# Kernel optimization log

Measured on AMD Instinct MI355X. Metric: run time of the kernel, lower is better.

Reference implementation:

```python
import jax, jax.numpy as jnp
import numpy as np

D, N, H, DK, DFF, L = 1024, 2048, 8, 128, 4096, 4
LAM = 1.0 / float(np.sqrt(DK))  # attention scale (layer.lam)


def setup_inputs() -> dict:
    key = jax.random.key(0)
    ks = jax.random.split(key, 6)
    s = 1.0 / float(np.sqrt(D))
    X = jax.random.normal(ks[0], (D, N), jnp.float32)
    Q = jax.random.normal(ks[1], (L, H, DK, D), jnp.float32) * s
    K = jax.random.normal(ks[2], (L, H, DK, D), jnp.float32) * s
    V = jax.random.normal(ks[3], (L, H, D, D), jnp.float32) * s
    W1 = jax.random.normal(ks[4], (L, DFF, D), jnp.float32) * s
    b1 = jnp.zeros((L, DFF, 1), jnp.float32)
    W2 = jax.random.normal(ks[5], (L, D, DFF), jnp.float32) * (1.0 / float(np.sqrt(DFF)))
    b2 = jnp.zeros((L, D, 1), jnp.float32)
    return {"X": X, "Q": Q, "K": K, "V": V, "W1": W1, "b1": b1, "W2": W2, "b2": b2}


def _layer(X, p):
    Q, K, V, W1, b1, W2, b2 = p
    # Batched multi-head attention; original loops heads and sums outputs.
    QX = jnp.einsum('hkd,dn->hkn', Q, X)          # [H, DK, N]
    KX = jnp.einsum('hkd,dn->hkn', K, X)          # [H, DK, N]
    scores = jnp.einsum('hkn,hkm->hnm', QX, KX) * LAM  # [H, N, N]
    A = jax.nn.softmax(scores, axis=1)            # torch softmax(dim=0) over [N, N]
    VX = jnp.einsum('hed,dn->hen', V, X)          # [H, D, N]
    Y = jnp.einsum('hen,hnm->em', VX, A)          # sum over heads -> [D, N]
    X = X + Y
    Hh = jax.nn.relu(W1 @ X + b1)                 # [DFF, N]
    return X + W2 @ Hh + b2


def reference(X, Q, K, V, W1, b1, W2, b2):
    def step(carry, p):
        return _layer(carry, p), None
    Xf, _ = jax.lax.scan(step, X, (Q, K, V, W1, b1, W2, b2))
    return Xf
```

## Files before the change

### kernel.cpp

```cpp
#include <hip/hip_runtime.h>

typedef unsigned short u16;
typedef _Float16 f16;
typedef _Float16 fh8 __attribute__((ext_vector_type(8)));
typedef float f32x4 __attribute__((ext_vector_type(4)));

#define cD   1024
#define cN   2048
#define cH   8
#define cDK  128
#define cDFF 4096
#define cL   4
#define LAM_ 0.08838834764831845f
#define QKSC 64.0f

__device__ __forceinline__ u16 f2h(float f) {
    union { f16 h; u16 u; } x; x.h = (f16)f; return x.u;
}
__device__ __forceinline__ float h2f(u16 u) {
    union { u16 u; f16 h; } x; x.u = u; return (float)x.h;
}
__device__ __forceinline__ void split_fh(float v, u16& h, u16& l) {
    h = f2h(v);
    l = f2h(v - h2f(h));
}

__device__ __forceinline__ void async_cp16(const u16* gsrc, u16* ldst) {
    __builtin_amdgcn_global_load_lds(
        (const __attribute__((address_space(1))) unsigned int*)gsrc,
        (__attribute__((address_space(3))) unsigned int*)(unsigned int)(unsigned long long)ldst,
        16, 0, 0);
}

__global__ void cast_split4(const float* __restrict__ s, u16* __restrict__ h,
                            u16* __restrict__ l, int n4, float sc) {
    int i = blockIdx.x * 256 + threadIdx.x;
    if (i < n4) {
        float4 v = ((const float4*)s)[i];
        v.x *= sc; v.y *= sc; v.z *= sc; v.w *= sc;
        ushort4 hh, ll;
        split_fh(v.x, hh.x, ll.x);
        split_fh(v.y, hh.y, ll.y);
        split_fh(v.z, hh.z, ll.z);
        split_fh(v.w, hh.w, ll.w);
        ((ushort4*)h)[i] = hh;
        if (l) ((ushort4*)l)[i] = ll;
    }
}

__global__ __launch_bounds__(256)
void transpose_f32(const float* __restrict__ in, float* __restrict__ out, int R, int C) {
    __shared__ float t[32][33];
    const int bx = blockIdx.x * 32;
    const int by = blockIdx.y * 32;
    const int tx = threadIdx.x & 31, ty = threadIdx.x >> 5;
#pragma unroll
    for (int yy = 0; yy < 32; yy += 8)
        t[ty + yy][tx] = in[(long)(by + ty + yy) * C + bx + tx];
    __syncthreads();
#pragma unroll
    for (int yy = 0; yy < 32; yy += 8)
        out[(long)(bx + ty + yy) * R + by + tx] = t[tx][ty + yy];
}

__global__ __launch_bounds__(256)
void softmax_rows(const float* __restrict__ S, u16* __restrict__ Ph) {
    const long base = (long)blockIdx.x * cN;
    const float4* s4 = (const float4*)(S + base);
    const int tid = threadIdx.x;
    float4 v0 = s4[tid];
    float4 v1 = s4[tid + 256];
    float mx = fmaxf(fmaxf(fmaxf(v0.x, v0.y), fmaxf(v0.z, v0.w)),
                     fmaxf(fmaxf(v1.x, v1.y), fmaxf(v1.z, v1.w)));
    __shared__ float rm[256], rl[256];
    rm[tid] = mx; __syncthreads();
    for (int w = 128; w > 0; w >>= 1) {
        if (tid < w) rm[tid] = fmaxf(rm[tid], rm[tid + w]);
        __syncthreads();
    }
    mx = rm[0];
    float l = __expf(v0.x - mx) + __expf(v0.y - mx) + __expf(v0.z - mx) + __expf(v0.w - mx)
            + __expf(v1.x - mx) + __expf(v1.y - mx) + __expf(v1.z - mx) + __expf(v1.w - mx);
    rl[tid] = l; __syncthreads();
    for (int w = 128; w > 0; w >>= 1) {
        if (tid < w) rl[tid] += rl[tid + w];
        __syncthreads();
    }
    const float inv = 1.0f / rl[0];
    ushort4 a, b;
    a.x = f2h(__expf(v0.x - mx) * inv);
    a.y = f2h(__expf(v0.y - mx) * inv);
    a.z = f2h(__expf(v0.z - mx) * inv);
    a.w = f2h(__expf(v0.w - mx) * inv);
    b.x = f2h(__expf(v1.x - mx) * inv);
    b.y = f2h(__expf(v1.y - mx) * inv);
    b.z = f2h(__expf(v1.z - mx) * inv);
    b.w = f2h(__expf(v1.w - mx) * inv);
    ((ushort4*)(Ph + base))[tid] = a;
    ((ushort4*)(Ph + base))[tid + 256] = b;
}

template<int ALO, int BLO, int DBUF>
__global__ __launch_bounds__(256)
void gemm_split(const u16* __restrict__ Ah, const u16* __restrict__ Al, int lda, long bsA,
                const u16* __restrict__ Bh, const u16* __restrict__ Bl, int ldb, long bsB,
                float* __restrict__ Cf, u16* __restrict__ Cbh, u16* __restrict__ Cbl,
                int ldc, long bsC,
                int M, int N, int K, int SK,
                float alpha, int mode, int relu, const float* __restrict__ biasN)
{
    const int g = blockIdx.z / SK;
    const int s = blockIdx.z % SK;
    const long za = (long)g * bsA + (long)s * K;
    const long zb = (long)g * bsB + (long)s * K;
    Ah += za; Bh += zb;
    if constexpr (ALO) Al += za;
    if constexpr (BLO) Bl += zb;
    if (s != 0) biasN = nullptr;

    __shared__ __align__(16) u16 Ash[128 * 32];
    __shared__ __align__(16) u16 Bsh[128 * 32];
    __shared__ __align__(16) u16 Asl[ALO ? 128 * 32 : 8];
    __shared__ __align__(16) u16 Bsl[BLO ? 128 * 32 : 8];
    __shared__ __align__(16) u16 Ash1[DBUF ? 128 * 32 : 8];
    __shared__ __align__(16) u16 Bsh1[DBUF ? 128 * 32 : 8];
    __shared__ __align__(16) u16 Ash2[DBUF ? 128 * 32 : 8];
    __shared__ __align__(16) u16 Bsh2[DBUF ? 128 * 32 : 8];

    const int tid  = threadIdx.x;
    const int lane = tid & 63;
    const int wave = tid >> 6;
    const int wm = (wave >> 1) * 64;
    const int wn = (wave & 1) * 64;

    const int nbx = gridDim.x;
    const int nwg = nbx * (int)gridDim.y;
    int wg = blockIdx.y * nbx + blockIdx.x;
    {
        const int qq = nwg >> 3, rr = nwg & 7;
        const int xcd = wg & 7, lid = wg >> 3;
        wg = (xcd < rr ? xcd * (qq + 1) : rr * (qq + 1) + (xcd - rr) * qq) + lid;
    }
    const int m0 = (wg / nbx) * 128;
    const int n0 = (wg % nbx) * 128;

    const int srow = lane >> 2;
    const int scol = (((lane & 3) ^ (srow & 3)) * 8);
    const int q = lane >> 4;
    const int r = lane & 15;
    const int fcol = ((q ^ (r & 3)) * 8);

    f32x4 acc[4][4];
#pragma unroll
    for (int i = 0; i < 4; ++i)
#pragma unroll
        for (int j = 0; j < 4; ++j)
            acc[i][j] = f32x4{0.f, 0.f, 0.f, 0.f};

    if constexpr (DBUF) {
        const int nt = K >> 5;
        auto stage = [&](u16* SA, u16* SB, int k0) {
#pragma unroll
            for (int p = 0; p < 2; ++p) {
                const int c = p * 4 + wave;
                const int grow = c * 16 + srow;
                async_cp16(Ah + (long)(m0 + grow) * lda + k0 + scol, SA + c * 512);
                async_cp16(Bh + (long)(n0 + grow) * ldb + k0 + scol, SB + c * 512);
            }
        };
        auto compute = [&](const u16* SA, const u16* SB) {
            fh8 af[4], bf[4];
#pragma unroll
            for (int i = 0; i < 4; ++i) af[i] = *(const fh8*)(SA + (wm + i * 16 + r) * 32 + fcol);
#pragma unroll
            for (int j = 0; j < 4; ++j) bf[j] = *(const fh8*)(SB + (wn + j * 16 + r) * 32 + fcol);
#pragma unroll
            for (int i = 0; i < 4; ++i)
#pragma unroll
                for (int j = 0; j < 4; ++j)
                    acc[i][j] = __builtin_amdgcn_mfma_f32_16x16x32_f16(af[i], bf[j], acc[i][j], 0, 0, 0);
        };
        auto step = [&](const u16* CA, const u16* CB, u16* PA, u16* PB, int pk) {
            if (pk < nt) {
                stage(PA, PB, pk * 32);
                asm volatile("s_waitcnt vmcnt(8)" ::: "memory");
            } else if (pk - 1 < nt) {
                asm volatile("s_waitcnt vmcnt(4)" ::: "memory");
            } else {
                asm volatile("s_waitcnt vmcnt(0)" ::: "memory");
            }
            __builtin_amdgcn_s_barrier();
            compute(CA, CB);
            __builtin_amdgcn_s_barrier();
        };

        stage(Ash,  Bsh,  0);
        stage(Ash1, Bsh1, 32);
        int t = 0;
        for (; t + 3 <= nt; t += 3) {
            step(Ash,  Bsh,  Ash2, Bsh2, t + 2);
            step(Ash1, Bsh1, Ash,  Bsh,  t + 3);
            step(Ash2, Bsh2, Ash1, Bsh1, t + 4);
        }
        if (nt - t == 2) {
            step(Ash,  Bsh,  Ash2, Bsh2, t + 2);
            step(Ash1, Bsh1, Ash2, Bsh2, t + 3);
        } else if (nt - t == 1) {
            step(Ash,  Bsh,  Ash2, Bsh2, t + 2);
        }
    } else {
        for (int k0 = 0; k0 < K; k0 += 32) {
#pragma unroll
            for (int p = 0; p < 2; ++p) {
                const int c = p * 4 + wave;
                const int grow = c * 16 + srow;
                const long aoff = (long)(m0 + grow) * lda + k0 + scol;
                const long boff = (long)(n0 + grow) * ldb + k0 + scol;
                async_cp16(Ah + aoff, Ash + c * 512);
                if constexpr (ALO) async_cp16(Al + aoff, Asl + c * 512);
                async_cp16(Bh + boff, Bsh + c * 512);
                if constexpr (BLO) async_cp16(Bl + boff, Bsl + c * 512);
            }
            __syncthreads();

            fh8 afh[4], afl[4], bfh[4], bfl[4];
#pragma unroll
            for (int i = 0; i < 4; ++i) {
                const int ra = (wm + i * 16 + r) * 32 + fcol;
                afh[i] = *(const fh8*)(Ash + ra);
                if constexpr (ALO) afl[i] = *(const fh8*)(Asl + ra);
            }
#pragma unroll
            for (int j = 0; j < 4; ++j) {
                const int rb = (wn + j * 16 + r) * 32 + fcol;
                bfh[j] = *(const fh8*)(Bsh + rb);
                if constexpr (BLO) bfl[j] = *(const fh8*)(Bsl + rb);
            }
#pragma unroll
            for (int i = 0; i < 4; ++i)
#pragma unroll
                for (int j = 0; j < 4; ++j) {
                    acc[i][j] = __builtin_amdgcn_mfma_f32_16x16x32_f16(afh[i], bfh[j], acc[i][j], 0, 0, 0);
                    if constexpr (BLO)
                        acc[i][j] = __builtin_amdgcn_mfma_f32_16x16x32_f16(afh[i], bfl[j], acc[i][j], 0, 0, 0);
                    if constexpr (ALO)
                        acc[i][j] = __builtin_amdgcn_mfma_f32_16x16x32_f16(afl[i], bfh[j], acc[i][j], 0, 0, 0);
                }
            __syncthreads();
        }
    }

#pragma unroll
    for (int i = 0; i < 4; ++i) {
#pragma unroll
        for (int j = 0; j < 4; ++j) {
            const int col = n0 + wn + j * 16 + r;
#pragma unroll
            for (int t = 0; t < 4; ++t) {
                const int row = m0 + wm + i * 16 + q * 4 + t;
                float v = acc[i][j][t] * alpha;
                if (biasN) v += biasN[col];
                if (relu)  v = fmaxf(v, 0.f);
                const long idx = (long)g * bsC + (long)row * ldc + col;
                if (mode == 0) {
                    if (Cbl) { u16 a, b; split_fh(v, a, b); Cbh[idx] = a; Cbl[idx] = b; }
                    else     { Cbh[idx] = f2h(v); }
                } else if (mode == 1) {
                    Cf[idx] = v;
                } else {
                    unsafeAtomicAdd(&Cf[idx], v);
                }
            }
        }
    }
}

static inline void launch_gemm(hipStream_t st, int split3,
                               const u16* Ah, const u16* Al, int lda, long bsA,
                               const u16* Bh, const u16* Bl, int ldb, long bsB,
                               float* Cf, u16* Cbh, u16* Cbl, int ldc, long bsC,
                               int M, int N, int K, int Gz, int SK,
                               float alpha, int mode, int relu, const float* biasN)
{
    dim3 grid(N / 128, M / 128, Gz * SK), block(256);
    if (split3)
        gemm_split<1, 1, 0><<<grid, block, 0, st>>>(Ah, Al, lda, bsA, Bh, Bl, ldb, bsB,
                                                    Cf, Cbh, Cbl, ldc, bsC,
                                                    M, N, K, SK, alpha, mode, relu, biasN);
    else
        gemm_split<0, 0, 1><<<grid, block, 0, st>>>(Ah, Al, lda, bsA, Bh, Bl, ldb, bsB,
                                                    Cf, Cbh, Cbl, ldc, bsC,
                                                    M, N, K, SK, alpha, mode, relu, biasN);
}

static inline void launch_cast(hipStream_t st, const float* s, u16* h, u16* l, long n,
                               float sc = 1.0f) {
    int n4 = (int)(n / 4);
    cast_split4<<<dim3((n4 + 255) / 256), dim3(256), 0, st>>>(s, h, l, n4, sc);
}

extern "C" void kernel_launch(void* const* d_in, const int* in_sizes, int n_in,
                              void* d_out, int out_size, void* d_ws, size_t ws_size,
                              hipStream_t stream)
{
    const float* Xin = (const float*)d_in[0];
    const float* Qw  = (const float*)d_in[1];
    const float* Kw  = (const float*)d_in[2];
    const float* Vw  = (const float*)d_in[3];
    const float* W1w = (const float*)d_in[4];
    const float* b1w = (const float*)d_in[5];
    const float* W2w = (const float*)d_in[6];
    const float* b2w = (const float*)d_in[7];
    float* Xout = (float*)d_out;

    int G = 1;
    if      (ws_size >= 402653184ull + 1048576) G = 8;
    else if (ws_size >= 218103808ull + 1048576) G = 4;
    else if (ws_size >= 125829120ull + 1048576) G = 2;

    char* base = (char*)d_ws;
    size_t off = 0;
    auto carve = [&](size_t bytes) {
        char* p = base + off; off = (off + bytes + 255) & ~(size_t)255; return p;
    };
    float* Xt     = (float*)carve((size_t)cN * cD * 4);
    u16*   XbT_h  = (u16*)carve((size_t)cN * cD * 2);
    u16*   XbT_l  = (u16*)carve((size_t)cN * cD * 2);
    u16*   QKXT_h = (u16*)carve((size_t)2 * cN * cD * 2);
    u16*   QKXT_l = (u16*)carve((size_t)2 * cN * cD * 2);
    u16*   W1_h   = QKXT_h;
    const size_t r2 = off;
    float* ST   = (float*)carve((size_t)G * cN * cN * 4);
    u16*   P_h  = (u16*)carve((size_t)G * cN * cN * 2);
    u16*   P_l  = (u16*)carve((size_t)G * cN * cN * 2);
    u16*   Vb_h = (u16*)carve((size_t)G * cD * cD * 2);
    u16*   Vb_l = (u16*)carve((size_t)G * cD * cD * 2);
    u16*   VX_h = (u16*)carve((size_t)G * cD * cN * 2);
    u16*   VX_l = (u16*)carve((size_t)G * cD * cN * 2);
    (void)P_l; (void)Vb_l; (void)VX_l;
    off = r2;
    u16*   QKb_h = (u16*)carve((size_t)2 * cH * cDK * cD * 2);
    u16*   QKb_l = (u16*)carve((size_t)2 * cH * cDK * cD * 2);
    off = r2;
    u16*   H1_h = (u16*)carve((size_t)cN * cDFF * 2);
    u16*   H1_l = (u16*)carve((size_t)cN * cDFF * 2);
    u16*   W2_h = (u16*)carve((size_t)cD * cDFF * 2);
    (void)H1_l;

    const u16* QXT_h = QKXT_h;
    const u16* QXT_l = QKXT_l;
    const u16* KXT_h = QKXT_h + (size_t)cN * cD;
    const u16* KXT_l = QKXT_l + (size_t)cN * cD;

    transpose_f32<<<dim3(cN / 32, cD / 32), dim3(256), 0, stream>>>(Xin, Xt, cD, cN);

    const int SKy = (G >= 4) ? 1 : (G == 2 ? 2 : 4);
    const float stalpha = LAM_ / (QKSC * QKSC);

    for (int l = 0; l < cL; ++l) {
        launch_cast(stream, Xt, XbT_h, XbT_l, (long)cN * cD);

        const long nQK = (long)cH * cDK * cD;
        launch_cast(stream, Qw + (long)l * nQK, QKb_h, QKb_l, nQK, QKSC);
        launch_cast(stream, Kw + (long)l * nQK, QKb_h + nQK, QKb_l + nQK, nQK, QKSC);

        launch_gemm(stream, 1, XbT_h, XbT_l, cD, 0,
                    QKb_h, QKb_l, cD, nQK,
                    nullptr, QKXT_h, QKXT_l, cD, (long)cN * cD,
                    cN, cD, cD, 2, 1, 1.f, 0, 0, nullptr);

        for (int g0 = 0; g0 < cH; g0 += G) {
            launch_gemm(stream, 1, KXT_h + (long)g0 * cDK, KXT_l + (long)g0 * cDK, cD, cDK,
                        QXT_h + (long)g0 * cDK, QXT_l + (long)g0 * cDK, cD, cDK,
                        ST, nullptr, nullptr, cN, (long)cN * cN,
                        cN, cN, cDK, G, 1, stalpha, 1, 0, nullptr);
            softmax_rows<<<dim3(G * cN), dim3(256), 0, stream>>>(ST, P_h);

            const long nV = (long)cD * cD;
            launch_cast(stream, Vw + ((long)l * cH + g0) * nV, Vb_h, nullptr, (long)G * nV);
            launch_gemm(stream, 0, Vb_h, nullptr, cD, nV,
                        XbT_h, nullptr, cD, 0,
                        nullptr, VX_h, nullptr, cN, (long)cD * cN,
                        cD, cN, cD, G, 1, 1.f, 0, 0, nullptr);
            launch_gemm(stream, 0, P_h, nullptr, cN, (long)cN * cN,
                        VX_h, nullptr, cN, (long)cD * cN,
                        Xt, nullptr, nullptr, cD, 0,
                        cN, cD, cN / SKy, G, SKy, 1.f, 3, 0, nullptr);
        }

        launch_cast(stream, Xt, XbT_h, nullptr, (long)cN * cD);
        const long nW = (long)cDFF * cD;
        launch_cast(stream, W1w + (long)l * nW, W1_h, nullptr, nW);
        launch_gemm(stream, 0, XbT_h, nullptr, cD, 0,
                    W1_h, nullptr, cD, 0,
                    nullptr, H1_h, nullptr, cDFF, 0,
                    cN, cDFF, cD, 1, 1, 1.f, 0, 1, b1w + (long)l * cDFF);
        launch_cast(stream, W2w + (long)l * nW, W2_h, nullptr, nW);
        launch_gemm(stream, 0, H1_h, nullptr, cDFF, 0,
                    W2_h, nullptr, cDFF, 0,
                    Xt, nullptr, nullptr, cD, 0,
                    cN, cD, cDFF / 4, 1, 4, 1.f, 3, 0, b2w + (long)l * cD);
    }

    transpose_f32<<<dim3(cD / 32, cN / 32), dim3(256), 0, stream>>>(Xt, Xout, cN, cD);

    (void)in_sizes; (void)n_in; (void)out_size;
}
```

Before: 2.031 ms.

## Add 256x256-tile triple-buffered fp16 GEMM for VX, PV and W2 products

Introduces a new 512-thread GEMM kernel with 256x256 output tiles, three-stage async LDS buffering, swizzled shared-memory layout and XCD-aware workgroup remapping. It is used for the VX and P·VX products when all heads are batched (G==8), and for the W2 projection with split-K raised to 8. Larger tiles raise arithmetic intensity and cut global/LDS traffic per FLOP. The cost is higher register and LDS pressure (8x4 accumulators per wave, 96KB LDS) and fewer workgroups per GEMM, which may reduce occupancy.

```diff
diff --git a/kernel.cpp b/kernel.cpp
--- a/kernel.cpp
+++ b/kernel.cpp
@@ -275,6 +275,126 @@
     }
 }
 
+__global__ __launch_bounds__(512, 2)
+void gemm_1p_256(const u16* __restrict__ Ah, int lda, long bsA,
+                 const u16* __restrict__ Bh, int ldb, long bsB,
+                 float* __restrict__ Cf, u16* __restrict__ Cbh, int ldc, long bsC,
+                 int K, int SK,
+                 float alpha, int mode, int relu, const float* __restrict__ biasN)
+{
+    const int g = blockIdx.z / SK;
+    const int s = blockIdx.z % SK;
+    Ah += (long)g * bsA + (long)s * K;
+    Bh += (long)g * bsB + (long)s * K;
+    if (s != 0) biasN = nullptr;
+
+    __shared__ __align__(16) u16 As0[256 * 32], Bs0[256 * 32];
+    __shared__ __align__(16) u16 As1[256 * 32], Bs1[256 * 32];
+    __shared__ __align__(16) u16 As2[256 * 32], Bs2[256 * 32];
+
+    const int tid  = threadIdx.x;
+    const int lane = tid & 63;
+    const int w    = tid >> 6;
+    const int wm   = (w >> 2) * 128;
+    const int wn   = (w & 3) * 64;
+
+    const int nbx = gridDim.x;
+    const int nwg = nbx * (int)gridDim.y;
+    int wg = blockIdx.y * nbx + blockIdx.x;
+    {
+        const int qq = nwg >> 3, rr = nwg & 7;
+        const int xcd = wg & 7, lid = wg >> 3;
+        wg = (xcd < rr ? xcd * (qq + 1) : rr * (qq + 1) + (xcd - rr) * qq) + lid;
+    }
+    const int m0 = (wg / nbx) * 256;
+    const int n0 = (wg % nbx) * 256;
+
+    const int srow = lane >> 2;
+    const int scol = ((((lane & 3) - (srow & 3) - (srow >> 2)) & 3) * 8);
+    const int q = lane >> 4;
+    const int r = lane & 15;
+    const int fcol = (((q + (r & 3) + (r >> 2)) & 3) * 8);
+
+    f32x4 acc[8][4];
+#pragma unroll
+    for (int i = 0; i < 8; ++i)
+#pragma unroll
+        for (int j = 0; j < 4; ++j)
+            acc[i][j] = f32x4{0.f, 0.f, 0.f, 0.f};
+
+    const int nt = K >> 5;
+    auto stage = [&](u16* SA, u16* SB, int k0) {
+#pragma unroll
+        for (int p = 0; p < 2; ++p) {
+            const int c = p * 8 + w;
+            const int grow = c * 16 + srow;
+            async_cp16(Ah + (long)(m0 + grow) * lda + k0 + scol, SA + c * 512);
+            async_cp16(Bh + (long)(n0 + grow) * ldb + k0 + scol, SB + c * 512);
+        }
+    };
+    auto compute = [&](const u16* SA, const u16* SB) {
+        fh8 af[8], bf[4];
+#pragma unroll
+        for (int i = 0; i < 8; ++i)
+            af[i] = *(const fh8*)(SA + ((wm >> 4) + i) * 512 + r * 32 + fcol);
+#pragma unroll
+        for (int j = 0; j < 4; ++j)
+            bf[j] = *(const fh8*)(SB + ((wn >> 4) + j) * 512 + r * 32 + fcol);
+#pragma unroll
+        for (int i = 0; i < 8; ++i)
+#pragma unroll
+            for (int j = 0; j < 4; ++j)
+                acc[i][j] = __builtin_amdgcn_mfma_f32_16x16x32_f16(af[i], bf[j], acc[i][j], 0, 0, 0);
+    };
+    auto step = [&](const u16* CA, const u16* CB, u16* PA, u16* PB, int pk) {
+        if (pk < nt) {
+            stage(PA, PB, pk * 32);
+            asm volatile("s_waitcnt vmcnt(8)" ::: "memory");
+        } else if (pk - 1 < nt) {
+            asm volatile("s_waitcnt vmcnt(4)" ::: "memory");
+        } else {
+            asm volatile("s_waitcnt vmcnt(0)" ::: "memory");
+        }
+        __builtin_amdgcn_s_barrier();
+        compute(CA, CB);
+        __builtin_amdgcn_s_barrier();
+    };
+
+    stage(As0, Bs0, 0);
+    stage(As1, Bs1, 32);
+    int t = 0;
+    for (; t + 3 <= nt; t += 3) {
+        step(As0, Bs0, As2, Bs2, t + 2);
+        step(As1, Bs1, As0, Bs0, t + 3);
+        step(As2, Bs2, As1, Bs1, t + 4);
+    }
+    if (nt - t == 2) {
+        step(As0, Bs0, As2, Bs2, t + 2);
+        step(As1, Bs1, As2, Bs2, t + 3);
+    } else if (nt - t == 1) {
+        step(As0, Bs0, As2, Bs2, t + 2);
+    }
+
+#pragma unroll
+    for (int i = 0; i < 8; ++i) {
+#pragma unroll
+        for (int j = 0; j < 4; ++j) {
+            const int col = n0 + wn + j * 16 + r;
+#pragma unroll
+            for (int t4 = 0; t4 < 4; ++t4) {
+                const int row = m0 + wm + i * 16 + q * 4 + t4;
+                float v = acc[i][j][t4] * alpha;
+                if (biasN) v += biasN[col];
+                if (relu)  v = fmaxf(v, 0.f);
+                const long idx = (long)g * bsC + (long)row * ldc + col;
+                if (mode == 0)      Cbh[idx] = f2h(v);
+                else if (mode == 1) Cf[idx] = v;
+                else                unsafeAtomicAdd(&Cf[idx], v);
+            }
+        }
+    }
+}
+
 static inline void launch_gemm(hipStream_t st, int split3,
                                const u16* Ah, const u16* Al, int lda, long bsA,
                                const u16* Bh, const u16* Bl, int ldb, long bsB,
@@ -291,6 +411,19 @@
         gemm_split<0, 0, 1><<<grid, block, 0, st>>>(Ah, Al, lda, bsA, Bh, Bl, ldb, bsB,
                                                     Cf, Cbh, Cbl, ldc, bsC,
                                                     M, N, K, SK, alpha, mode, relu, biasN);
+}
+
+static inline void launch_gemm256(hipStream_t st,
+                                  const u16* Ah, int lda, long bsA,
+                                  const u16* Bh, int ldb, long bsB,
+                                  float* Cf, u16* Cbh, int ldc, long bsC,
+                                  int M, int N, int K, int Gz, int SK,
+                                  float alpha, int mode, int relu, const float* biasN)
+{
+    dim3 grid(N / 256, M / 256, Gz * SK), block(512);
+    gemm_1p_256<<<grid, block, 0, st>>>(Ah, lda, bsA, Bh, ldb, bsB,
+                                        Cf, Cbh, ldc, bsC,
+                                        K, SK, alpha, mode, relu, biasN);
 }
 
 static inline void launch_cast(hipStream_t st, const float* s, u16* h, u16* l, long n,
@@ -378,14 +511,25 @@
 
             const long nV = (long)cD * cD;
             launch_cast(stream, Vw + ((long)l * cH + g0) * nV, Vb_h, nullptr, (long)G * nV);
-            launch_gemm(stream, 0, Vb_h, nullptr, cD, nV,
-                        XbT_h, nullptr, cD, 0,
-                        nullptr, VX_h, nullptr, cN, (long)cD * cN,
-                        cD, cN, cD, G, 1, 1.f, 0, 0, nullptr);
-            launch_gemm(stream, 0, P_h, nullptr, cN, (long)cN * cN,
-                        VX_h, nullptr, cN, (long)cD * cN,
-                        Xt, nullptr, nullptr, cD, 0,
-                        cN, cD, cN / SKy, G, SKy, 1.f, 3, 0, nullptr);
+            if (G == 8) {
+                launch_gemm256(stream, Vb_h, cD, nV,
+                               XbT_h, cD, 0,
+                               nullptr, VX_h, cN, (long)cD * cN,
+                               cD, cN, cD, G, 1, 1.f, 0, 0, nullptr);
+                launch_gemm256(stream, P_h, cN, (long)cN * cN,
+                               VX_h, cN, (long)cD * cN,
+                               Xt, nullptr, cD, 0,
+                               cN, cD, cN, G, 1, 1.f, 3, 0, nullptr);
+            } else {
+                launch_gemm(stream, 0, Vb_h, nullptr, cD, nV,
+                            XbT_h, nullptr, cD, 0,
+                            nullptr, VX_h, nullptr, cN, (long)cD * cN,
+                            cD, cN, cD, G, 1, 1.f, 0, 0, nullptr);
+                launch_gemm(stream, 0, P_h, nullptr, cN, (long)cN * cN,
+                            VX_h, nullptr, cN, (long)cD * cN,
+                            Xt, nullptr, nullptr, cD, 0,
+                            cN, cD, cN / SKy, G, SKy, 1.f, 3, 0, nullptr);
+            }
         }
 
         launch_cast(stream, Xt, XbT_h, nullptr, (long)cN * cD);
@@ -396,10 +540,10 @@
                     nullptr, H1_h, nullptr, cDFF, 0,
                     cN, cDFF, cD, 1, 1, 1.f, 0, 1, b1w + (long)l * cDFF);
         launch_cast(stream, W2w + (long)l * nW, W2_h, nullptr, nW);
-        launch_gemm(stream, 0, H1_h, nullptr, cDFF, 0,
-                    W2_h, nullptr, cDFF, 0,
-                    Xt, nullptr, nullptr, cD, 0,
-                    cN, cD, cDFF / 4, 1, 4, 1.f, 3, 0, b2w + (long)l * cD);
+        launch_gemm256(stream, H1_h, cDFF, 0,
+                       W2_h, cDFF, 0,
+                       Xt, nullptr, cD, 0,
+                       cN, cD, cDFF / 8, 1, 8, 1.f, 3, 0, b2w + (long)l * cD);
     }
 
     transpose_f32<<<dim3(cD / 32, cN / 32), dim3(256), 0, stream>>>(Xt, Xout, cN, cD);
```

After: 2.558 ms. 25.9% more time.

## Store attention scores in fp16 and interleave heads for single split-K PV GEMM

Applied to the files above, without the earlier changes.

The scores GEMM now writes fp16 instead of fp32, which halves the score write and read traffic in the softmax. When eight heads are batched, the softmax and VX outputs are laid out with heads interleaved along the contraction dimension. This lets the head-summed P·VX product run as one GEMM with K = 8·N and split-K 4, instead of a batched GEMM over heads with atomic accumulation. It risks lower precision in the fp16 scores (values scaled by LAM/64² could lose accuracy) and changes the GEMM shapes.

```diff
diff --git a/kernel.cpp b/kernel.cpp
--- a/kernel.cpp
+++ b/kernel.cpp
@@ -64,14 +64,19 @@
 }
 
 __global__ __launch_bounds__(256)
-void softmax_rows(const float* __restrict__ S, u16* __restrict__ Ph) {
-    const long base = (long)blockIdx.x * cN;
-    const float4* s4 = (const float4*)(S + base);
+void softmax_rows(const u16* __restrict__ S16, u16* __restrict__ Ph, long ldm, long zoff) {
+    const int bid = blockIdx.x;
+    const int z = bid >> 11;
+    const int m = bid & (cN - 1);
+    const long rbase = (long)bid * cN;
+    const long wbase = (long)m * ldm + (long)z * zoff;
     const int tid = threadIdx.x;
-    float4 v0 = s4[tid];
-    float4 v1 = s4[tid + 256];
-    float mx = fmaxf(fmaxf(fmaxf(v0.x, v0.y), fmaxf(v0.z, v0.w)),
-                     fmaxf(fmaxf(v1.x, v1.y), fmaxf(v1.z, v1.w)));
+    ushort4 h0 = ((const ushort4*)(S16 + rbase))[tid];
+    ushort4 h1 = ((const ushort4*)(S16 + rbase))[tid + 256];
+    float v0x = h2f(h0.x), v0y = h2f(h0.y), v0z = h2f(h0.z), v0w = h2f(h0.w);
+    float v1x = h2f(h1.x), v1y = h2f(h1.y), v1z = h2f(h1.z), v1w = h2f(h1.w);
+    float mx = fmaxf(fmaxf(fmaxf(v0x, v0y), fmaxf(v0z, v0w)),
+                     fmaxf(fmaxf(v1x, v1y), fmaxf(v1z, v1w)));
     __shared__ float rm[256], rl[256];
     rm[tid] = mx; __syncthreads();
     for (int w = 128; w > 0; w >>= 1) {
@@ -79,8 +84,8 @@
         __syncthreads();
     }
     mx = rm[0];
-    float l = __expf(v0.x - mx) + __expf(v0.y - mx) + __expf(v0.z - mx) + __expf(v0.w - mx)
-            + __expf(v1.x - mx) + __expf(v1.y - mx) + __expf(v1.z - mx) + __expf(v1.w - mx);
+    float l = __expf(v0x - mx) + __expf(v0y - mx) + __expf(v0z - mx) + __expf(v0w - mx)
+            + __expf(v1x - mx) + __expf(v1y - mx) + __expf(v1z - mx) + __expf(v1w - mx);
     rl[tid] = l; __syncthreads();
     for (int w = 128; w > 0; w >>= 1) {
         if (tid < w) rl[tid] += rl[tid + w];
@@ -88,16 +93,16 @@
     }
     const float inv = 1.0f / rl[0];
     ushort4 a, b;
-    a.x = f2h(__expf(v0.x - mx) * inv);
-    a.y = f2h(__expf(v0.y - mx) * inv);
-    a.z = f2h(__expf(v0.z - mx) * inv);
-    a.w = f2h(__expf(v0.w - mx) * inv);
-    b.x = f2h(__expf(v1.x - mx) * inv);
-    b.y = f2h(__expf(v1.y - mx) * inv);
-    b.z = f2h(__expf(v1.z - mx) * inv);
-    b.w = f2h(__expf(v1.w - mx) * inv);
-    ((ushort4*)(Ph + base))[tid] = a;
-    ((ushort4*)(Ph + base))[tid + 256] = b;
+    a.x = f2h(__expf(v0x - mx) * inv);
+    a.y = f2h(__expf(v0y - mx) * inv);
+    a.z = f2h(__expf(v0z - mx) * inv);
+    a.w = f2h(__expf(v0w - mx) * inv);
+    b.x = f2h(__expf(v1x - mx) * inv);
+    b.y = f2h(__expf(v1y - mx) * inv);
+    b.z = f2h(__expf(v1z - mx) * inv);
+    b.w = f2h(__expf(v1w - mx) * inv);
+    ((ushort4*)(Ph + wbase))[tid] = a;
+    ((ushort4*)(Ph + wbase))[tid + 256] = b;
 }
 
 template<int ALO, int BLO, int DBUF>
@@ -330,7 +335,7 @@
     u16*   QKXT_l = (u16*)carve((size_t)2 * cN * cD * 2);
     u16*   W1_h   = QKXT_h;
     const size_t r2 = off;
-    float* ST   = (float*)carve((size_t)G * cN * cN * 4);
+    u16*   ST16 = (u16*)carve((size_t)G * cN * cN * 4);
     u16*   P_h  = (u16*)carve((size_t)G * cN * cN * 2);
     u16*   P_l  = (u16*)carve((size_t)G * cN * cN * 2);
     u16*   Vb_h = (u16*)carve((size_t)G * cD * cD * 2);
@@ -372,20 +377,36 @@
         for (int g0 = 0; g0 < cH; g0 += G) {
             launch_gemm(stream, 1, KXT_h + (long)g0 * cDK, KXT_l + (long)g0 * cDK, cD, cDK,
                         QXT_h + (long)g0 * cDK, QXT_l + (long)g0 * cDK, cD, cDK,
-                        ST, nullptr, nullptr, cN, (long)cN * cN,
-                        cN, cN, cDK, G, 1, stalpha, 1, 0, nullptr);
-            softmax_rows<<<dim3(G * cN), dim3(256), 0, stream>>>(ST, P_h);
+                        nullptr, ST16, nullptr, cN, (long)cN * cN,
+                        cN, cN, cDK, G, 1, stalpha, 0, 0, nullptr);
+            if (G == 8)
+                softmax_rows<<<dim3(G * cN), dim3(256), 0, stream>>>(ST16, P_h,
+                                                                     (long)G * cN, (long)cN);
+            else
+                softmax_rows<<<dim3(G * cN), dim3(256), 0, stream>>>(ST16, P_h,
+                                                                     (long)cN, (long)cN * cN);
 
             const long nV = (long)cD * cD;
             launch_cast(stream, Vw + ((long)l * cH + g0) * nV, Vb_h, nullptr, (long)G * nV);
-            launch_gemm(stream, 0, Vb_h, nullptr, cD, nV,
-                        XbT_h, nullptr, cD, 0,
-                        nullptr, VX_h, nullptr, cN, (long)cD * cN,
-                        cD, cN, cD, G, 1, 1.f, 0, 0, nullptr);
-            launch_gemm(stream, 0, P_h, nullptr, cN, (long)cN * cN,
-                        VX_h, nullptr, cN, (long)cD * cN,
-                        Xt, nullptr, nullptr, cD, 0,
-                        cN, cD, cN / SKy, G, SKy, 1.f, 3, 0, nullptr);
+            if (G == 8) {
+                launch_gemm(stream, 0, Vb_h, nullptr, cD, nV,
+                            XbT_h, nullptr, cD, 0,
+                            nullptr, VX_h, nullptr, G * cN, (long)cN,
+                            cD, cN, cD, G, 1, 1.f, 0, 0, nullptr);
+                launch_gemm(stream, 0, P_h, nullptr, G * cN, 0,
+                            VX_h, nullptr, G * cN, 0,
+                            Xt, nullptr, nullptr, cD, 0,
+                            cN, cD, G * cN / 4, 1, 4, 1.f, 3, 0, nullptr);
+            } else {
+                launch_gemm(stream, 0, Vb_h, nullptr, cD, nV,
+                            XbT_h, nullptr, cD, 0,
+                            nullptr, VX_h, nullptr, cN, (long)cD * cN,
+                            cD, cN, cD, G, 1, 1.f, 0, 0, nullptr);
+                launch_gemm(stream, 0, P_h, nullptr, cN, (long)cN * cN,
+                            VX_h, nullptr, cN, (long)cD * cN,
+                            Xt, nullptr, nullptr, cD, 0,
+                            cN, cD, cN / SKy, G, SKy, 1.f, 3, 0, nullptr);
+            }
         }
 
         launch_cast(stream, Xt, XbT_h, nullptr, (long)cN * cD);
```

New measurement: 1.943 ms. -4.4%, faster.
